# Performance work log

Hardware: AMD Instinct MI355X
Metric: run time of the kernel (lower is better)

Reference implementation:

```python
import jax, jax.numpy as jnp
import numpy as np

B, S, D_MODEL, D_HEAD = 8, 2048, 1024, 128
MAX_ROUNDS = 3
THRESH = 0.1
SCALE = 1.0 / np.sqrt(float(D_HEAD))


def setup_inputs() -> dict:
    key = jax.random.key(0)
    ks = jax.random.split(key, 12)

    def lin(k, out_d, in_d):
        # torch Linear weight layout [out, in], y = x @ W.T + b
        return (jax.random.normal(k, (out_d, in_d), jnp.float32) / np.sqrt(float(in_d))).astype(jnp.float32)

    thesis_w = lin(ks[3], D_HEAD, D_HEAD)
    return {
        "x": jax.random.normal(ks[0], (B, S, D_MODEL), jnp.float32),
        "wq": lin(ks[1], D_HEAD, D_MODEL),
        "wk": lin(ks[2], D_HEAD, D_MODEL),
        "wv": lin(ks[4], D_HEAD, D_MODEL),
        "thesis_w": thesis_w,  # antithesis weight is -thesis_w per __init__
        "thesis_b": 0.02 * jax.random.normal(ks[5], (D_HEAD,), jnp.float32),
        "anti_b": 0.02 * jax.random.normal(ks[6], (D_HEAD,), jnp.float32),
        "s_w1": lin(ks[7], D_HEAD, 3 * D_HEAD),
        "s_b1": jnp.zeros((D_HEAD,), jnp.float32),
        "s_w2": lin(ks[8], D_HEAD, D_HEAD),
        "s_b2": jnp.zeros((D_HEAD,), jnp.float32),
        "g_w": lin(ks[9], 1, 2 * D_HEAD),
        "g_b": jnp.zeros((1,), jnp.float32),
    }


def reference(x, wq, wk, wv, thesis_w, thesis_b, anti_b, s_w1, s_b1, s_w2, s_b2, g_w, g_b):
    # q/k/v projections (no bias)
    q = jnp.einsum("bsm,hm->bsh", x, wq)
    k = jnp.einsum("bsm,hm->bsh", x, wk)
    v = jnp.einsum("bsm,hm->bsh", x, wv)

    attn = jax.nn.softmax(jnp.einsum("bqh,bkh->bqk", q, k) * SCALE, axis=-1)
    # dropout is identity at eval time
    cur = jnp.einsum("bqk,bkh->bqh", attn, v)  # [B,S,Dh]

    # attn_weights and v never change across rounds, so thesis/antithesis are
    # round-invariant: compute the context projections once.
    context = cur
    thesis = context @ thesis_w.T + thesis_b
    anti = context @ (-thesis_w).T + anti_b  # antithesis weight = -thesis weight

    active = jnp.ones((B, S), dtype=bool)
    for _ in range(MAX_ROUNDS):
        # emulate `if not active_mask.any(): break` under jit
        any_active = jnp.any(active)
        am = active[..., None].astype(x.dtype)
        at, aa, ac = thesis * am, anti * am, cur * am

        h = jax.nn.relu(jnp.concatenate([at, aa, ac], axis=-1) @ s_w1.T + s_b1)
        synth = h @ s_w2.T + s_b2
        gate = jax.nn.sigmoid(jnp.concatenate([ac, synth], axis=-1) @ g_w.T + g_b)
        update = gate * (synth - ac) * 0.1
        new = cur + update  # applied to ALL tokens, matching original

        stable = jnp.linalg.norm(update, axis=-1) < THRESH  # new - cur == update
        cur = jnp.where(any_active, new, cur)
        active = jnp.where(any_active, active & ~stable, active)
    return cur
```

## Files before the change

### kernel.cpp

```cpp
#include <hip/hip_runtime.h>
#include <hip/hip_bf16.h>

#define B_   8
#define S_   2048
#define DM   1024
#define DH   128
#define BS_  16384
#define SCALE_  0.08838834764831845f
#define SCALE2_ 0.12751744f

typedef unsigned short u16;
typedef unsigned int   u32;
typedef _Float16 half8 __attribute__((ext_vector_type(8)));
typedef __bf16   bf16x8 __attribute__((ext_vector_type(8)));
typedef float    f32x4 __attribute__((ext_vector_type(4)));
typedef u32      u32x4 __attribute__((ext_vector_type(4)));

union H8 { u32x4 v; u32 u[4]; half8 h; bf16x8 b; };

__device__ __forceinline__ float bf2f(u16 u) {
    union { u32 i; float f; } w; w.i = ((u32)u) << 16; return w.f;
}
__device__ __forceinline__ void unpack8(uint4 v, float* f) {
    f[0] = bf2f(v.x & 0xffff); f[1] = bf2f(v.x >> 16);
    f[2] = bf2f(v.y & 0xffff); f[3] = bf2f(v.y >> 16);
    f[4] = bf2f(v.z & 0xffff); f[5] = bf2f(v.z >> 16);
    f[6] = bf2f(v.w & 0xffff); f[7] = bf2f(v.w >> 16);
}
__device__ __forceinline__ float ldE(const void* b, size_t i, int isbf16) {
    return isbf16 ? bf2f(((const u16*)b)[i]) : ((const float*)b)[i];
}
__device__ __forceinline__ void ld8(const void* b, size_t i, int isbf16, float* f) {
    if (isbf16) {
        unpack8(*(const uint4*)((const u16*)b + i), f);
    } else {
        float4 a = *(const float4*)((const float*)b + i);
        float4 c = *(const float4*)((const float*)b + i + 4);
        f[0] = a.x; f[1] = a.y; f[2] = a.z; f[3] = a.w;
        f[4] = c.x; f[5] = c.y; f[6] = c.z; f[7] = c.w;
    }
}
__device__ __forceinline__ u32 f2pk(float v) {
    _Float16 h = (_Float16)v;
    _Float16 l = (_Float16)(v - (float)h);
    union { _Float16 f; u16 u; } a, b; a.f = h; b.f = l;
    return ((u32)a.u << 16) | (u32)b.u;
}
__device__ __forceinline__ void split8(const float* f, u32x4& hi, u32x4& lo) {
    u32 H[8], L[8];
#pragma unroll
    for (int j = 0; j < 8; ++j) {
        _Float16 h = (_Float16)f[j];
        _Float16 l = (_Float16)(f[j] - (float)h);
        union { _Float16 x; u16 u; } a, b; a.x = h; b.x = l;
        H[j] = a.u; L[j] = b.u;
    }
    hi = (u32x4){H[0] | (H[1] << 16), H[2] | (H[3] << 16), H[4] | (H[5] << 16), H[6] | (H[7] << 16)};
    lo = (u32x4){L[0] | (L[1] << 16), L[2] | (L[3] << 16), L[4] | (L[5] << 16), L[6] | (L[7] << 16)};
}
__device__ __forceinline__ u32 permHI(u32 eB, u32 eA) { return __builtin_amdgcn_perm(eB, eA, 0x07060302u); }
__device__ __forceinline__ u16 f2h(float v) { union { _Float16 f; u16 u; } a; a.f = (_Float16)v; return a.u; }
__device__ __forceinline__ float h2f(u16 u) { union { _Float16 f; u16 u; } a; a.u = u; return (float)a.f; }

__global__ void init_kernel(const void* x, int* flag, int* active, int* counts) {
    int i = blockIdx.x * 256 + threadIdx.x;
    if (i < BS_) active[i] = 1;
    if (i < 4) counts[i] = (i == 0) ? BS_ : 0;
    if (i == 0) {
        const u16* w = (const u16*)x;
        int sane = 0;
        for (int t = 0; t < 256; ++t) {
            int e = (w[2 * t] >> 7) & 0xFF;
            if (e >= 100 && e <= 135) ++sane;
        }
        *flag = (sane >= 192) ? 1 : 0;
    }
}

__global__ __launch_bounds__(256) void prepack_w_kernel(
    const void* __restrict__ wq, const void* __restrict__ wk, const void* __restrict__ wv,
    const int* __restrict__ flag, u32x4* __restrict__ wpk)
{
    const int isb = *flag;
    const int gid = blockIdx.x * 256 + threadIdx.x;
    const int l  = gid & 63;
    const int t  = (gid >> 6) & 7;
    const int ks = (gid >> 9) & 31;
    const int z  = gid >> 14;
    const void* W = (z == 0) ? wq : (z == 1) ? wk : wv;
    const int row = 16 * t + (l & 15);
    const int k0  = ks * 32 + 8 * (l >> 4);
    const size_t base = ((((size_t)z * 32 + ks) * 16) + 2 * t) * 64 + l;
    if (isb) {
        uint4 v = *(const uint4*)((const u16*)W + (size_t)row * DM + k0);
        wpk[base] = (u32x4){v.x, v.y, v.z, v.w};
    } else {
        float f[8];
        ld8(W, (size_t)row * DM + k0, 0, f);
        u32x4 hi, lo;
        split8(f, hi, lo);
        wpk[base]      = hi;
        wpk[base + 64] = lo;
    }
}

__global__ __launch_bounds__(256) void qkv_kernel(
    const void* __restrict__ x, const u32x4* __restrict__ wpk,
    const int* __restrict__ flag, u32* __restrict__ qout,
    u32x4* __restrict__ kfrag, u32x4* __restrict__ vfrag)
{
    const int isb = *flag;
    const int z = blockIdx.z;
    const int bx = blockIdx.x;
    const int m0 = ((bx & 7) * 32 + (bx >> 3)) * 64;
    const int tid = threadIdx.x;
    const int wave = tid >> 6, lane = tid & 63;
    const int qd = lane >> 4, c = lane & 15;

    __shared__ u32x4 WLraw[2][16][64];
    u32x4 (*WLb)[2][8][64] = (u32x4(*)[2][8][64])WLraw;
    u32x4 (*WLf)[8][2][64] = (u32x4(*)[8][2][64])WLraw;
    u16 (*TS)[136] = (u16(*)[136])WLraw;

    const u32x4* wz = wpk + (size_t)z * (32 * 16 * 64);
    const size_t arow = (size_t)(m0 + wave * 16 + c) * DM + 8 * qd;

#define STAGE2(i_, b_)                                                            \
    {                                                                             \
        _Pragma("unroll")                                                         \
        for (int _j = 0; _j < 4; ++_j) {                                          \
            const int _g = wave * 4 + _j, _ksub = _g >> 3, _t = _g & 7;           \
            __builtin_amdgcn_global_load_lds(                                     \
                (const __attribute__((address_space(1))) u32*)(                   \
                    wz + ((size_t)(2 * (i_) + _ksub) * 16 + 2 * _t) * 64 + lane), \
                (__attribute__((address_space(3))) u32*)&WLb[b_][_ksub][_t][0],   \
                16, 0, 0);                                                        \
        }                                                                         \
    }
#define STAGE_W(ks_, b_)                                                          \
    {                                                                             \
        const u32x4* _src = wz + ((size_t)(ks_) * 16 + 4 * wave) * 64 + lane;     \
        _Pragma("unroll")                                                         \
        for (int _j = 0; _j < 4; ++_j) {                                          \
            __builtin_amdgcn_global_load_lds(                                     \
                (const __attribute__((address_space(1))) u32*)(_src + _j * 64),   \
                (__attribute__((address_space(3))) u32*)&WLf[b_][2 * wave + (_j >> 1)][_j & 1][0], \
                16, 0, 0);                                                        \
        }                                                                         \
    }

    f32x4 acc[8] = {};

    if (isb) {
        const u16* xb = (const u16*)x;
        uint4 A0 = *(const uint4*)(xb + arow);
        uint4 A1 = *(const uint4*)(xb + arow + 32);
        STAGE2(0, 0);
        uint4 A0n = *(const uint4*)(xb + arow + 64);
        uint4 A1n = *(const uint4*)(xb + arow + 96);
        __syncthreads();
        for (int i = 0; i < 16; ++i) {
            const int cb = i & 1;
            if (i + 1 < 16) STAGE2(i + 1, cb ^ 1);
            H8 Ah0; Ah0.v = (u32x4){A0.x, A0.y, A0.z, A0.w};
            H8 Ah1; Ah1.v = (u32x4){A1.x, A1.y, A1.z, A1.w};
#pragma unroll
            for (int t = 0; t < 8; ++t) {
                H8 bh; bh.v = WLb[cb][0][t][lane];
                acc[t] = __builtin_amdgcn_mfma_f32_16x16x32_bf16(Ah0.b, bh.b, acc[t], 0, 0, 0);
            }
#pragma unroll
            for (int t = 0; t < 8; ++t) {
                H8 bh; bh.v = WLb[cb][1][t][lane];
                acc[t] = __builtin_amdgcn_mfma_f32_16x16x32_bf16(Ah1.b, bh.b, acc[t], 0, 0, 0);
            }
            A0 = A0n; A1 = A1n;
            if (i + 2 < 16) {
                A0n = *(const uint4*)(xb + arow + (size_t)(i + 2) * 64);
                A1n = *(const uint4*)(xb + arow + (size_t)(i + 2) * 64 + 32);
            }
            __syncthreads();
        }
    } else {
        float Ar[8], Arn[8];
        ld8(x, arow, 0, Ar);
        STAGE_W(0, 0);
        ld8(x, arow + 32, 0, Arn);
        __syncthreads();
        for (int ks = 0; ks < 32; ++ks) {
            const int cb = ks & 1;
            if (ks + 1 < 32) STAGE_W(ks + 1, cb ^ 1);
            H8 Ah, Al;
            split8(Ar, Ah.v, Al.v);
#pragma unroll
            for (int t = 0; t < 8; ++t) {
                H8 bh, bl;
                bh.v = WLf[cb][t][0][lane]; bl.v = WLf[cb][t][1][lane];
                acc[t] = __builtin_amdgcn_mfma_f32_16x16x32_f16(Al.h, bh.h, acc[t], 0, 0, 0);
                acc[t] = __builtin_amdgcn_mfma_f32_16x16x32_f16(Ah.h, bl.h, acc[t], 0, 0, 0);
                acc[t] = __builtin_amdgcn_mfma_f32_16x16x32_f16(Ah.h, bh.h, acc[t], 0, 0, 0);
            }
#pragma unroll
            for (int j = 0; j < 8; ++j) Ar[j] = Arn[j];
            if (ks + 2 < 32) ld8(x, arow + (size_t)(ks + 2) * 32, 0, Arn);
            __syncthreads();
        }
    }
#undef STAGE2
#undef STAGE_W

    if (z == 0) {
#pragma unroll
        for (int r = 0; r < 4; ++r) {
            const int row = m0 + wave * 16 + qd * 4 + r;
            u32* op = qout + (size_t)row * DH + c;
#pragma unroll
            for (int t = 0; t < 8; ++t) op[t * 16] = f2pk(acc[t][r]);
        }
    } else {
#pragma unroll
        for (int t = 0; t < 8; ++t)
#pragma unroll
            for (int r = 0; r < 4; ++r)
                TS[wave * 16 + qd * 4 + r][16 * t + c] = f2h(acc[t][r]);
        __syncthreads();
        if (z == 1) {
#pragma unroll
            for (int i = 0; i < 4; ++i) {
                const int f = tid + 256 * i;
                const int lf = f & 63, ks = (f >> 6) & 3, sub = f >> 8;
                const int key = sub * 16 + (lf & 15);
                const int d0  = ks * 32 + 8 * (lf >> 4);
                u32 w[4];
#pragma unroll
                for (int q = 0; q < 4; ++q)
                    w[q] = (u32)TS[key][d0 + 2 * q] | ((u32)TS[key][d0 + 2 * q + 1] << 16);
                kfrag[((size_t)(m0 / 16 + sub) * 4 + ks) * 64 + lf] = (u32x4){w[0], w[1], w[2], w[3]};
            }
        } else {
#pragma unroll
            for (int i = 0; i < 4; ++i) {
                const int f = tid + 256 * i;
                const int lf = f & 63, t = (f >> 6) & 7, sub = f >> 9;
                const int kb2 = sub * 32 + 8 * (lf >> 4);
                const int dh  = 16 * t + (lf & 15);
                u32 w[4];
#pragma unroll
                for (int q = 0; q < 4; ++q)
                    w[q] = (u32)TS[kb2 + 2 * q][dh] | ((u32)TS[kb2 + 2 * q + 1][dh] << 16);
                vfrag[((size_t)(m0 / 32 + sub) * 8 + t) * 64 + lf] = (u32x4){w[0], w[1], w[2], w[3]};
            }
        }
    }
}

template <bool WRITE_PARTIAL>
__device__ __forceinline__ void attn_body(
    const u32* qp, const u32x4* __restrict__ kfrag, const u32x4* __restrict__ vfrag,
    u16* outO, u16* outL, float* cur,
    int b, int q0, int kt0, int kt1, int part)
{
    const int tid = threadIdx.x;
    const int wave = tid >> 6, lane = tid & 63;
    const int qd = lane >> 4, c = lane & 15;

    __shared__ u16 PB[4][531];

    H8 Qh[4];
    {
        const u32* qr = qp + ((size_t)b * S_ + q0 + wave * 16 + c) * DH;
#pragma unroll
        for (int ks = 0; ks < 4; ++ks) {
            uint4 e0 = *(const uint4*)(qr + ks * 32 + qd * 8);
            uint4 e1 = *(const uint4*)(qr + ks * 32 + qd * 8 + 4);
            Qh[ks].u[0] = permHI(e0.y, e0.x); Qh[ks].u[1] = permHI(e0.w, e0.z);
            Qh[ks].u[2] = permHI(e1.y, e1.x); Qh[ks].u[3] = permHI(e1.w, e1.z);
        }
    }

    f32x4 O[8] = {};
    float lsum[4] = {};

    const u32x4* kb0 = kfrag + (size_t)b * 128 * 256;
    const u32x4* vb0 = vfrag + (size_t)b * 64 * 512;

    for (int kt = kt0; kt < kt1; ++kt) {
        const u32x4* kf = kb0 + (size_t)kt * 512;
        const u32x4* vf = vb0 + (size_t)kt * 512;

        f32x4 S0 = {}, S1 = {};
#pragma unroll
        for (int ks = 0; ks < 4; ++ks) {
            H8 kh;
            kh.v = kf[ks * 64 + lane];
            S0 = __builtin_amdgcn_mfma_f32_16x16x32_f16(Qh[ks].h, kh.h, S0, 0, 0, 0);
            kh.v = kf[256 + ks * 64 + lane];
            S1 = __builtin_amdgcn_mfma_f32_16x16x32_f16(Qh[ks].h, kh.h, S1, 0, 0, 0);
        }

        u16* pw = PB[wave];
#pragma unroll
        for (int r = 0; r < 4; ++r) {
            float e0 = exp2f(fmaf(S0[r], SCALE2_, -4.0f));
            float e1 = exp2f(fmaf(S1[r], SCALE2_, -4.0f));
            lsum[r] += e0 + e1;
            pw[(4 * qd + r) * 33 + c]      = f2h(e0);
            pw[(4 * qd + r) * 33 + 16 + c] = f2h(e1);
        }

        u16 e[8];
#pragma unroll
        for (int j = 0; j < 8; ++j) e[j] = pw[c * 33 + 8 * qd + j];
        H8 Ph;
        Ph.u[0] = (u32)e[0] | ((u32)e[1] << 16);
        Ph.u[1] = (u32)e[2] | ((u32)e[3] << 16);
        Ph.u[2] = (u32)e[4] | ((u32)e[5] << 16);
        Ph.u[3] = (u32)e[6] | ((u32)e[7] << 16);

#pragma unroll
        for (int t = 0; t < 8; ++t) {
            H8 vh;
            vh.v = vf[t * 64 + lane];
            O[t] = __builtin_amdgcn_mfma_f32_16x16x32_f16(Ph.h, vh.h, O[t], 0, 0, 0);
        }
    }

    if (WRITE_PARTIAL) {
        float lred[4];
#pragma unroll
        for (int r = 0; r < 4; ++r) {
            float l = lsum[r];
            l += __shfl_xor(l, 1); l += __shfl_xor(l, 2);
            l += __shfl_xor(l, 4); l += __shfl_xor(l, 8);
            lred[r] = l;
        }
        const size_t rb = (size_t)b * S_ + q0 + wave * 16 + 4 * qd;
        u16* Op = outO + (size_t)part * ((size_t)BS_ * DH);
#pragma unroll
        for (int t = 0; t < 8; ++t)
#pragma unroll
            for (int r = 0; r < 4; ++r)
                Op[(rb + r) * DH + t * 16 + c] = f2h(O[t][r]);
        if (c == 0) {
            u16* lp = outL + (size_t)part * BS_;
#pragma unroll
            for (int r = 0; r < 4; ++r) lp[rb + r] = f2h(lred[r]);
        }
    } else {
        float linv[4];
#pragma unroll
        for (int r = 0; r < 4; ++r) {
            float l = lsum[r];
            l += __shfl_xor(l, 1); l += __shfl_xor(l, 2);
            l += __shfl_xor(l, 4); l += __shfl_xor(l, 8);
            linv[r] = 1.0f / l;
        }
        const size_t rb = (size_t)b * S_ + q0 + wave * 16 + 4 * qd;
#pragma unroll
        for (int t = 0; t < 8; ++t)
#pragma unroll
            for (int r = 0; r < 4; ++r)
                cur[(rb + r) * DH + t * 16 + c] = O[t][r] * linv[r];
    }
}

__global__ __launch_bounds__(256) void attn_kernel(
    const u32* qp, const u32x4* __restrict__ kfrag, const u32x4* __restrict__ vfrag, float* cur)
{
    const int rid = blockIdx.x + 32 * blockIdx.y;
    attn_body<false>(qp, kfrag, vfrag, nullptr, nullptr, cur,
                     rid & 7, ((rid >> 3) & 31) * 64, 0, S_ / 32, 0);
}

__global__ __launch_bounds__(256) void attn_split_kernel(
    const u32* qp, const u32x4* __restrict__ kfrag, const u32x4* __restrict__ vfrag,
    u16* __restrict__ Opart, u16* __restrict__ lpart)
{
    const int rid = blockIdx.x + 32 * (blockIdx.y + 8 * blockIdx.z);
    const int b    = rid & 7;
    const int qx   = (rid >> 3) & 31;
    const int part = rid >> 8;
    const int quart = S_ / 128;
    attn_body<true>(qp, kfrag, vfrag, Opart, lpart, nullptr,
                    b, qx * 64, part * quart, (part + 1) * quart, part);
}

__global__ __launch_bounds__(256) void combine_kernel(
    const u16* __restrict__ Opart, const u16* __restrict__ lpart,
    float* __restrict__ cur)
{
    const size_t N1 = (size_t)BS_ * DH;
    const size_t i0 = ((size_t)blockIdx.x * 256 + threadIdx.x) * 16;
    const int row = (int)(i0 >> 7);
    const float lt = h2f(lpart[row]) + h2f(lpart[BS_ + row])
                   + h2f(lpart[2 * BS_ + row]) + h2f(lpart[3 * BS_ + row]);
    const float linv = 1.0f / lt;
    float acc[16] = {};
#pragma unroll
    for (int p = 0; p < 4; ++p) {
        const u16* op = Opart + (size_t)p * N1 + i0;
        uint4 v0 = *(const uint4*)op;
        uint4 v1 = *(const uint4*)(op + 8);
        const u32 w[8] = {v0.x, v0.y, v0.z, v0.w, v1.x, v1.y, v1.z, v1.w};
#pragma unroll
        for (int j = 0; j < 8; ++j) {
            acc[2 * j]     += h2f((u16)(w[j] & 0xffff));
            acc[2 * j + 1] += h2f((u16)(w[j] >> 16));
        }
    }
#pragma unroll
    for (int t = 0; t < 4; ++t)
        *(float4*)(cur + i0 + t * 4) = make_float4(
            acc[4*t] * linv, acc[4*t+1] * linv, acc[4*t+2] * linv, acc[4*t+3] * linv);
}

__global__ __launch_bounds__(256) void prepack_rw_kernel(
    const void* __restrict__ tw, const void* __restrict__ w1, const void* __restrict__ w2,
    const int* __restrict__ flag, u32x4* __restrict__ pk)
{
    const int isb = *flag;
    const int gid = blockIdx.x * 256 + threadIdx.x;
    const int l = gid & 63, t = (gid >> 6) & 7, ks = (gid >> 9) & 3, mat = gid >> 11;
    const int row = 16 * t + (l & 15);
    const int k0  = ks * 32 + 8 * (l >> 4);
    float f[8];
    if (mat == 0)      ld8(tw, (size_t)row * DH + k0, isb, f);
    else if (mat <= 3) ld8(w1, (size_t)row * 384 + (mat - 1) * 128 + k0, isb, f);
    else               ld8(w2, (size_t)row * DH + k0, isb, f);
    u32x4 hi, lo;
    split8(f, hi, lo);
    const size_t base = (((size_t)mat * 4 + ks) * 16 + 2 * t) * 64 + l;
    pk[base] = hi; pk[base + 64] = lo;
}

struct Afrag { H8 h[4], l[4]; };
__device__ __forceinline__ void splitA(const float (&A)[4][8], Afrag& F) {
#pragma unroll
    for (int ks = 0; ks < 4; ++ks) split8(A[ks], F.h[ks].v, F.l[ks].v);
}

__global__ __launch_bounds__(256) void round_kernel(
    const float* cur0, const float* curr,
    const u32x4* __restrict__ pk,
    const void* __restrict__ tb, const void* __restrict__ ab,
    const void* __restrict__ b1, const void* __restrict__ b2,
    const void* __restrict__ gw, const void* __restrict__ gb,
    const int* __restrict__ flag, int* active, int* counts, int r,
    float* cur_out, void* dout)
{
    const int isb = *flag;
    const int tok0 = blockIdx.x * 32;
    const int tid = threadIdx.x;
    const bool last = (dout != nullptr);

    if (counts[r] <= 0) {
        if (last) {
            for (int e = tid; e < 32 * DH; e += 256) {
                size_t idx = (size_t)tok0 * DH + e;
                float v = curr[idx];
                if (isb) ((__hip_bfloat16*)dout)[idx] = __float2bfloat16(v);
                else     ((float*)dout)[idx] = v;
            }
        }
        return;
    }

    const int wave = tid >> 6, lane = tid & 63;
    const int qd = lane >> 4, c = lane & 15;
    const int rowg = wave >> 1, colh = wave & 1;

    __shared__ u32x4 WB[2][4][8][64];
    __shared__ u16 TS[32][132];
    __shared__ float actS[32], tbS[128], abS[128], b1S[128], b2S[128], gwS[256];
    __shared__ int blkcnt;

    auto stageB = [&](int mat, int buf) {
#pragma unroll
        for (int j = 0; j < 8; ++j) {
            const int g = wave * 8 + j, ks = g >> 3, t = g & 7;
            __builtin_amdgcn_global_load_lds(
                (const __attribute__((address_space(1))) u32*)(
                    pk + (((size_t)mat * 4 + ks) * 16 + 2 * t) * 64 + lane),
                (__attribute__((address_space(3))) u32*)&WB[buf][ks][t][0],
                16, 0, 0);
        }
    };
    auto stageF = [&](int mat, int h, int buf) {
#pragma unroll
        for (int j = 0; j < 8; ++j) {
            const int g = wave * 8 + j, kl = g >> 4, p = (g >> 3) & 1, t = g & 7;
            __builtin_amdgcn_global_load_lds(
                (const __attribute__((address_space(1))) u32*)(
                    pk + (((size_t)mat * 4 + 2 * h + kl) * 16 + 2 * t + p) * 64 + lane),
                (__attribute__((address_space(3))) u32*)&WB[buf][kl * 2 + p][t][0],
                16, 0, 0);
        }
    };
    auto gemmB = [&](const Afrag& F, int buf, f32x4 (&acc)[4]) {
#pragma unroll
        for (int ks = 0; ks < 4; ++ks)
#pragma unroll
            for (int tl = 0; tl < 4; ++tl) {
                H8 bh; bh.v = WB[buf][ks][4 * colh + tl][lane];
                acc[tl] = __builtin_amdgcn_mfma_f32_16x16x32_f16(F.l[ks].h, bh.h, acc[tl], 0, 0, 0);
                acc[tl] = __builtin_amdgcn_mfma_f32_16x16x32_f16(F.h[ks].h, bh.h, acc[tl], 0, 0, 0);
            }
    };
    auto gemmFh = [&](const Afrag& F, int h, int buf, f32x4 (&acc)[4]) {
#pragma unroll
        for (int kl = 0; kl < 2; ++kl) {
            const int ks = 2 * h + kl;
#pragma unroll
            for (int tl = 0; tl < 4; ++tl) {
                H8 bh, bl;
                bh.v = WB[buf][kl * 2][4 * colh + tl][lane];
                bl.v = WB[buf][kl * 2 + 1][4 * colh + tl][lane];
                acc[tl] = __builtin_amdgcn_mfma_f32_16x16x32_f16(F.l[ks].h, bh.h, acc[tl], 0, 0, 0);
                acc[tl] = __builtin_amdgcn_mfma_f32_16x16x32_f16(F.h[ks].h, bl.h, acc[tl], 0, 0, 0);
                acc[tl] = __builtin_amdgcn_mfma_f32_16x16x32_f16(F.h[ks].h, bh.h, acc[tl], 0, 0, 0);
            }
        }
    };
    auto STAGE = [&](int mat, int buf) { if (isb) stageB(mat, buf); else stageF(mat, 0, buf); };
    auto GEMM = [&](int mat, const Afrag& F, int buf, f32x4 (&acc)[4]) {
        if (isb) {
            gemmB(F, buf, acc);
        } else {
            gemmFh(F, 0, buf, acc);
            __syncthreads();
            stageF(mat, 1, buf);
            __syncthreads();
            gemmFh(F, 1, buf, acc);
        }
    };

    STAGE(0, 0);
    if (tid < 32) actS[tid] = active[tok0 + tid] ? 1.0f : 0.0f;
    if (tid < 128) {
        tbS[tid] = ldE(tb, tid, isb); abS[tid] = ldE(ab, tid, isb);
        b1S[tid] = ldE(b1, tid, isb); b2S[tid] = ldE(b2, tid, isb);
    }
    gwS[tid] = ldE(gw, tid, isb);
    if (tid == 0) blkcnt = 0;
    const float gbf = ldE(gb, 0, isb);

    const int rowl = 16 * rowg + c;
    const int hr   = 16 * rowg + 4 * qd;

    float A1[4][8];
    {
        const float* cr = cur0 + (size_t)(tok0 + rowl) * DH;
#pragma unroll
        for (int ks = 0; ks < 4; ++ks) {
            *(float4*)&A1[ks][0] = *(const float4*)(cr + ks * 32 + 8 * qd);
            *(float4*)&A1[ks][4] = *(const float4*)(cr + ks * 32 + 8 * qd + 4);
        }
    }
    Afrag FA; splitA(A1, FA);
    __syncthreads();

    STAGE(1, 1);
    {
        f32x4 accT[4] = {};
        GEMM(0, FA, 0, accT);
#pragma unroll
        for (int tl = 0; tl < 4; ++tl)
#pragma unroll
            for (int rr = 0; rr < 4; ++rr)
                TS[hr + rr][16 * (4 * colh + tl) + c] = f2h(accT[tl][rr]);
    }
    __syncthreads();

    STAGE(2, 0);
    f32x4 acc1[4] = {};
    const float am_r = actS[rowl];
    {
        float Ac[4][8];
#pragma unroll
        for (int ks = 0; ks < 4; ++ks)
#pragma unroll
            for (int j = 0; j < 8; ++j) {
                const int k = ks * 32 + 8 * qd + j;
                Ac[ks][j] = (h2f(TS[rowl][k]) + tbS[k]) * am_r;
            }
        Afrag FC; splitA(Ac, FC);
        GEMM(1, FC, 1, acc1);
    }
    __syncthreads();

    STAGE(3, 1);
    {
        float Ac[4][8];
#pragma unroll
        for (int ks = 0; ks < 4; ++ks)
#pragma unroll
            for (int j = 0; j < 8; ++j) {
                const int k = ks * 32 + 8 * qd + j;
                Ac[ks][j] = (abS[k] - h2f(TS[rowl][k])) * am_r;
            }
        Afrag FC; splitA(Ac, FC);
        GEMM(2, FC, 0, acc1);
    }
    __syncthreads();

    STAGE(4, 0);
    {
        float Ac[4][8];
        const float* cr = curr + (size_t)(tok0 + rowl) * DH;
#pragma unroll
        for (int ks = 0; ks < 4; ++ks) {
            float4 a0 = *(const float4*)(cr + ks * 32 + 8 * qd);
            float4 a1 = *(const float4*)(cr + ks * 32 + 8 * qd + 4);
            Ac[ks][0] = a0.x * am_r; Ac[ks][1] = a0.y * am_r;
            Ac[ks][2] = a0.z * am_r; Ac[ks][3] = a0.w * am_r;
            Ac[ks][4] = a1.x * am_r; Ac[ks][5] = a1.y * am_r;
            Ac[ks][6] = a1.z * am_r; Ac[ks][7] = a1.w * am_r;
        }
        Afrag FC; splitA(Ac, FC);
        GEMM(3, FC, 1, acc1);
    }
#pragma unroll
    for (int tl = 0; tl < 4; ++tl)
#pragma unroll
        for (int rr = 0; rr < 4; ++rr) {
            const int col = 16 * (4 * colh + tl) + c;
            TS[hr + rr][col] = f2h(fmaxf(acc1[tl][rr] + b1S[col], 0.0f));
        }
    __syncthreads();

    {
        float Ac[4][8];
#pragma unroll
        for (int ks = 0; ks < 4; ++ks)
#pragma unroll
            for (int j = 0; j < 8; ++j)
                Ac[ks][j] = h2f(TS[rowl][ks * 32 + 8 * qd + j]);
        Afrag FC; splitA(Ac, FC);
        f32x4 acc2[4] = {};
        GEMM(4, FC, 0, acc2);
        __syncthreads();
#pragma unroll
        for (int tl = 0; tl < 4; ++tl)
#pragma unroll
            for (int rr = 0; rr < 4; ++rr) {
                const int col = 16 * (4 * colh + tl) + c;
                TS[hr + rr][col] = f2h(acc2[tl][rr] + b2S[col]);
            }
    }
    __syncthreads();

    const int tok = tid >> 3, d0 = (tid & 7) * 16;
    const float am = actS[tok];
    const float* cp = curr + (size_t)(tok0 + tok) * DH + d0;
    float cv[16];
#pragma unroll
    for (int t = 0; t < 4; ++t) {
        float4 vv = *(const float4*)(cp + t * 4);
        cv[t * 4] = vv.x; cv[t * 4 + 1] = vv.y; cv[t * 4 + 2] = vv.z; cv[t * 4 + 3] = vv.w;
    }
    float srow[16];
#pragma unroll
    for (int e = 0; e < 16; ++e) srow[e] = h2f(TS[tok][d0 + e]);
    float gp = 0.0f;
#pragma unroll
    for (int e = 0; e < 16; ++e)
        gp += cv[e] * am * gwS[d0 + e] + srow[e] * gwS[128 + d0 + e];
    gp += __shfl_xor(gp, 1, 8);
    gp += __shfl_xor(gp, 2, 8);
    gp += __shfl_xor(gp, 4, 8);
    const float gate = 1.0f / (1.0f + __expf(-(gp + gbf)));
    float ss = 0.0f; float up[16];
#pragma unroll
    for (int e = 0; e < 16; ++e) {
        float u = gate * (srow[e] - cv[e] * am) * 0.1f;
        up[e] = u; ss += u * u;
    }
    ss += __shfl_xor(ss, 1, 8);
    ss += __shfl_xor(ss, 2, 8);
    ss += __shfl_xor(ss, 4, 8);
    const bool stable = sqrtf(ss) < 0.1f;

    if (last) {
        size_t off = (size_t)(tok0 + tok) * DH + d0;
        if (isb) {
            __hip_bfloat16* op = (__hip_bfloat16*)dout + off;
#pragma unroll
            for (int e = 0; e < 16; ++e) op[e] = __float2bfloat16(cv[e] + up[e]);
        } else {
            float* op = (float*)dout + off;
#pragma unroll
            for (int t = 0; t < 4; ++t)
                *(float4*)(op + t * 4) = make_float4(cv[t * 4] + up[t * 4], cv[t * 4 + 1] + up[t * 4 + 1],
                                                     cv[t * 4 + 2] + up[t * 4 + 2], cv[t * 4 + 3] + up[t * 4 + 3]);
        }
    } else {
        float* op = cur_out + (size_t)(tok0 + tok) * DH + d0;
#pragma unroll
        for (int t = 0; t < 4; ++t)
            *(float4*)(op + t * 4) = make_float4(cv[t * 4] + up[t * 4], cv[t * 4 + 1] + up[t * 4 + 1],
                                                 cv[t * 4 + 2] + up[t * 4 + 2], cv[t * 4 + 3] + up[t * 4 + 3]);
    }
    const int newact = (am > 0.0f && !stable) ? 1 : 0;
    if ((tid & 7) == 0) {
        active[tok0 + tok] = newact;
        if (newact) atomicAdd(&blkcnt, 1);
    }
    __syncthreads();
    if (tid == 0 && blkcnt > 0) atomicAdd(&counts[r + 1], blkcnt);
}

extern "C" void kernel_launch(void* const* d_in, const int* in_sizes, int n_in,
                              void* d_out, int out_size, void* d_ws, size_t ws_size,
                              hipStream_t stream) {
    const void* x  = d_in[0];
    const void* wq = d_in[1];
    const void* wk = d_in[2];
    const void* wv = d_in[3];
    const void* tw = d_in[4];
    const void* tb = d_in[5];
    const void* ab = d_in[6];
    const void* w1 = d_in[7];
    const void* b1 = d_in[8];
    const void* w2 = d_in[9];
    const void* b2 = d_in[10];
    const void* gw = d_in[11];
    const void* gb = d_in[12];

    u32* ws = (u32*)d_ws;
    const size_t N1 = (size_t)BS_ * DH;
    u32* qp = ws;
    u32* kp = ws + N1;
    u32* vp = ws + 2 * N1;
    int* active = (int*)(ws + 3 * N1);
    int* counts = active + BS_;
    int* flag   = counts + 4;
    float* cur0  = (float*)qp;
    float* cur_r = (float*)kp;
    u16* Opart16 = (u16*)(ws + 3 * N1 + 32768);
    u16* lpart16 = (u16*)(ws + 5 * N1 + 32768);
    const bool big_ws = ws_size >= (size_t)42300000;
    u32x4* wpk = (u32x4*)(ws + 3 * N1 + 32768);
    u32x4* pkRW = (u32x4*)vp;
    u32x4* kfragP = (u32x4*)kp;
    u32x4* vfragP = (u32x4*)vp;

    init_kernel<<<dim3(BS_ / 256), 256, 0, stream>>>(x, flag, active, counts);
    prepack_w_kernel<<<dim3(192), 256, 0, stream>>>(wq, wk, wv, flag, wpk);
    qkv_kernel<<<dim3(BS_ / 64, 1, 3), 256, 0, stream>>>(x, wpk, flag, qp, kfragP, vfragP);
    if (big_ws) {
        attn_split_kernel<<<dim3(S_ / 64, B_, 4), 256, 0, stream>>>(qp, kfragP, vfragP, Opart16, lpart16);
        combine_kernel<<<dim3(512), 256, 0, stream>>>(Opart16, lpart16, cur0);
    } else {
        attn_kernel<<<dim3(S_ / 64, B_), 256, 0, stream>>>(qp, kfragP, vfragP, cur0);
    }
    prepack_rw_kernel<<<dim3(40), 256, 0, stream>>>(tw, w1, w2, flag, pkRW);
    round_kernel<<<dim3(BS_ / 32), 256, 0, stream>>>(
        cur0, cur0, pkRW, tb, ab, b1, b2, gw, gb, flag, active, counts, 0, cur_r, nullptr);
    round_kernel<<<dim3(BS_ / 32), 256, 0, stream>>>(
        cur0, cur_r, pkRW, tb, ab, b1, b2, gw, gb, flag, active, counts, 1, cur_r, nullptr);
    round_kernel<<<dim3(BS_ / 32), 256, 0, stream>>>(
        cur0, cur_r, pkRW, tb, ab, b1, b2, gw, gb, flag, active, counts, 2, cur_r, d_out);
}
```

Before: 256.5 us.

## Load QKV weight fragments directly from global into registers, drop LDS staging

Removes the double-buffered global_load_lds staging of packed weight fragments and the per-iteration __syncthreads in the QKV projection kernel. Each wave now reads its B fragments straight from global memory (L2) into registers, with software register prefetch in the bf16 path and no prefetch in the fp32 split path. This removes barrier and LDS traffic, but every wave in a block now fetches the same weights redundantly from cache. It also raises register pressure, and the fp32 path loses latency hiding for its loads.

Result: slower. 287.3 us (+12.0%).

```diff
diff --git a/kernel.cpp b/kernel.cpp
--- a/kernel.cpp
+++ b/kernel.cpp
@@ -117,97 +117,55 @@
     const int wave = tid >> 6, lane = tid & 63;
     const int qd = lane >> 4, c = lane & 15;
 
-    __shared__ u32x4 WLraw[2][16][64];
-    u32x4 (*WLb)[2][8][64] = (u32x4(*)[2][8][64])WLraw;
-    u32x4 (*WLf)[8][2][64] = (u32x4(*)[8][2][64])WLraw;
-    u16 (*TS)[136] = (u16(*)[136])WLraw;
+    __shared__ u16 TS[64][136];
 
     const u32x4* wz = wpk + (size_t)z * (32 * 16 * 64);
     const size_t arow = (size_t)(m0 + wave * 16 + c) * DM + 8 * qd;
 
-#define STAGE2(i_, b_)                                                            \
-    {                                                                             \
-        _Pragma("unroll")                                                         \
-        for (int _j = 0; _j < 4; ++_j) {                                          \
-            const int _g = wave * 4 + _j, _ksub = _g >> 3, _t = _g & 7;           \
-            __builtin_amdgcn_global_load_lds(                                     \
-                (const __attribute__((address_space(1))) u32*)(                   \
-                    wz + ((size_t)(2 * (i_) + _ksub) * 16 + 2 * _t) * 64 + lane), \
-                (__attribute__((address_space(3))) u32*)&WLb[b_][_ksub][_t][0],   \
-                16, 0, 0);                                                        \
-        }                                                                         \
-    }
-#define STAGE_W(ks_, b_)                                                          \
-    {                                                                             \
-        const u32x4* _src = wz + ((size_t)(ks_) * 16 + 4 * wave) * 64 + lane;     \
-        _Pragma("unroll")                                                         \
-        for (int _j = 0; _j < 4; ++_j) {                                          \
-            __builtin_amdgcn_global_load_lds(                                     \
-                (const __attribute__((address_space(1))) u32*)(_src + _j * 64),   \
-                (__attribute__((address_space(3))) u32*)&WLf[b_][2 * wave + (_j >> 1)][_j & 1][0], \
-                16, 0, 0);                                                        \
-        }                                                                         \
-    }
-
     f32x4 acc[8] = {};
 
     if (isb) {
         const u16* xb = (const u16*)x;
-        uint4 A0 = *(const uint4*)(xb + arow);
-        uint4 A1 = *(const uint4*)(xb + arow + 32);
-        STAGE2(0, 0);
-        uint4 A0n = *(const uint4*)(xb + arow + 64);
-        uint4 A1n = *(const uint4*)(xb + arow + 96);
-        __syncthreads();
-        for (int i = 0; i < 16; ++i) {
-            const int cb = i & 1;
-            if (i + 1 < 16) STAGE2(i + 1, cb ^ 1);
-            H8 Ah0; Ah0.v = (u32x4){A0.x, A0.y, A0.z, A0.w};
-            H8 Ah1; Ah1.v = (u32x4){A1.x, A1.y, A1.z, A1.w};
-#pragma unroll
-            for (int t = 0; t < 8; ++t) {
-                H8 bh; bh.v = WLb[cb][0][t][lane];
-                acc[t] = __builtin_amdgcn_mfma_f32_16x16x32_bf16(Ah0.b, bh.b, acc[t], 0, 0, 0);
-            }
-#pragma unroll
-            for (int t = 0; t < 8; ++t) {
-                H8 bh; bh.v = WLb[cb][1][t][lane];
-                acc[t] = __builtin_amdgcn_mfma_f32_16x16x32_bf16(Ah1.b, bh.b, acc[t], 0, 0, 0);
-            }
-            A0 = A0n; A1 = A1n;
-            if (i + 2 < 16) {
-                A0n = *(const uint4*)(xb + arow + (size_t)(i + 2) * 64);
-                A1n = *(const uint4*)(xb + arow + (size_t)(i + 2) * 64 + 32);
-            }
-            __syncthreads();
+        uint4 Ab = *(const uint4*)(xb + arow);
+        H8 Bc[8];
+#pragma unroll
+        for (int t = 0; t < 8; ++t) Bc[t].v = wz[(size_t)(2 * t) * 64 + lane];
+        for (int ks = 0; ks < 32; ++ks) {
+            H8 Bn[8];
+            uint4 An;
+            if (ks + 1 < 32) {
+#pragma unroll
+                for (int t = 0; t < 8; ++t)
+                    Bn[t].v = wz[((size_t)(ks + 1) * 16 + 2 * t) * 64 + lane];
+                An = *(const uint4*)(xb + arow + (size_t)(ks + 1) * 32);
+            }
+            H8 Ah; Ah.v = (u32x4){Ab.x, Ab.y, Ab.z, Ab.w};
+#pragma unroll
+            for (int t = 0; t < 8; ++t)
+                acc[t] = __builtin_amdgcn_mfma_f32_16x16x32_bf16(Ah.b, Bc[t].b, acc[t], 0, 0, 0);
+            if (ks + 1 < 32) {
+#pragma unroll
+                for (int t = 0; t < 8; ++t) Bc[t] = Bn[t];
+                Ab = An;
+            }
         }
     } else {
-        float Ar[8], Arn[8];
-        ld8(x, arow, 0, Ar);
-        STAGE_W(0, 0);
-        ld8(x, arow + 32, 0, Arn);
-        __syncthreads();
+        float Ar[8];
         for (int ks = 0; ks < 32; ++ks) {
-            const int cb = ks & 1;
-            if (ks + 1 < 32) STAGE_W(ks + 1, cb ^ 1);
+            ld8(x, arow + (size_t)ks * 32, 0, Ar);
             H8 Ah, Al;
             split8(Ar, Ah.v, Al.v);
 #pragma unroll
             for (int t = 0; t < 8; ++t) {
                 H8 bh, bl;
-                bh.v = WLf[cb][t][0][lane]; bl.v = WLf[cb][t][1][lane];
+                bh.v = wz[((size_t)ks * 16 + 2 * t) * 64 + lane];
+                bl.v = wz[((size_t)ks * 16 + 2 * t + 1) * 64 + lane];
                 acc[t] = __builtin_amdgcn_mfma_f32_16x16x32_f16(Al.h, bh.h, acc[t], 0, 0, 0);
                 acc[t] = __builtin_amdgcn_mfma_f32_16x16x32_f16(Ah.h, bl.h, acc[t], 0, 0, 0);
                 acc[t] = __builtin_amdgcn_mfma_f32_16x16x32_f16(Ah.h, bh.h, acc[t], 0, 0, 0);
             }
-#pragma unroll
-            for (int j = 0; j < 8; ++j) Ar[j] = Arn[j];
-            if (ks + 2 < 32) ld8(x, arow + (size_t)(ks + 2) * 32, 0, Arn);
-            __syncthreads();
-        }
-    }
-#undef STAGE2
-#undef STAGE_W
+        }
+    }
 
     if (z == 0) {
 #pragma unroll
```

## Halve QKV block row tile and split output columns across waves

Applied to the files above, without the earlier changes.

The QKV projection kernel now processes 32 rows per block instead of 64. The four waves form a 2x2 grid over rows and the two 64-column halves, and the grid is doubled to match. Each wave keeps half as many accumulators, which lowers register pressure and doubles the number of blocks to improve occupancy and load balance. In exchange, the weight tiles staged in LDS are reused across fewer rows, so global weight traffic per output roughly doubles.

Result: slower. 298.9 us (+16.5%).

```diff
diff --git a/kernel.cpp b/kernel.cpp
--- a/kernel.cpp
+++ b/kernel.cpp
@@ -112,10 +112,11 @@
     const int isb = *flag;
     const int z = blockIdx.z;
     const int bx = blockIdx.x;
-    const int m0 = ((bx & 7) * 32 + (bx >> 3)) * 64;
+    const int m0 = ((bx & 7) * 64 + (bx >> 3)) * 32;
     const int tid = threadIdx.x;
     const int wave = tid >> 6, lane = tid & 63;
     const int qd = lane >> 4, c = lane & 15;
+    const int rowg = wave >> 1, colh = wave & 1;
 
     __shared__ u32x4 WLraw[2][16][64];
     u32x4 (*WLb)[2][8][64] = (u32x4(*)[2][8][64])WLraw;
@@ -123,7 +124,8 @@
     u16 (*TS)[136] = (u16(*)[136])WLraw;
 
     const u32x4* wz = wpk + (size_t)z * (32 * 16 * 64);
-    const size_t arow = (size_t)(m0 + wave * 16 + c) * DM + 8 * qd;
+    const int rowl = 16 * rowg + c;
+    const size_t arow = (size_t)(m0 + rowl) * DM + 8 * qd;
 
 #define STAGE2(i_, b_)                                                            \
     {                                                                             \
@@ -149,7 +151,7 @@
         }                                                                         \
     }
 
-    f32x4 acc[8] = {};
+    f32x4 acc[4] = {};
 
     if (isb) {
         const u16* xb = (const u16*)x;
@@ -165,14 +167,14 @@
             H8 Ah0; Ah0.v = (u32x4){A0.x, A0.y, A0.z, A0.w};
             H8 Ah1; Ah1.v = (u32x4){A1.x, A1.y, A1.z, A1.w};
 #pragma unroll
-            for (int t = 0; t < 8; ++t) {
-                H8 bh; bh.v = WLb[cb][0][t][lane];
-                acc[t] = __builtin_amdgcn_mfma_f32_16x16x32_bf16(Ah0.b, bh.b, acc[t], 0, 0, 0);
-            }
-#pragma unroll
-            for (int t = 0; t < 8; ++t) {
-                H8 bh; bh.v = WLb[cb][1][t][lane];
-                acc[t] = __builtin_amdgcn_mfma_f32_16x16x32_bf16(Ah1.b, bh.b, acc[t], 0, 0, 0);
+            for (int tl = 0; tl < 4; ++tl) {
+                H8 bh; bh.v = WLb[cb][0][4 * colh + tl][lane];
+                acc[tl] = __builtin_amdgcn_mfma_f32_16x16x32_bf16(Ah0.b, bh.b, acc[tl], 0, 0, 0);
+            }
+#pragma unroll
+            for (int tl = 0; tl < 4; ++tl) {
+                H8 bh; bh.v = WLb[cb][1][4 * colh + tl][lane];
+                acc[tl] = __builtin_amdgcn_mfma_f32_16x16x32_bf16(Ah1.b, bh.b, acc[tl], 0, 0, 0);
             }
             A0 = A0n; A1 = A1n;
             if (i + 2 < 16) {
@@ -193,12 +195,13 @@
             H8 Ah, Al;
             split8(Ar, Ah.v, Al.v);
 #pragma unroll
-            for (int t = 0; t < 8; ++t) {
+            for (int tl = 0; tl < 4; ++tl) {
                 H8 bh, bl;
-                bh.v = WLf[cb][t][0][lane]; bl.v = WLf[cb][t][1][lane];
-                acc[t] = __builtin_amdgcn_mfma_f32_16x16x32_f16(Al.h, bh.h, acc[t], 0, 0, 0);
-                acc[t] = __builtin_amdgcn_mfma_f32_16x16x32_f16(Ah.h, bl.h, acc[t], 0, 0, 0);
-                acc[t] = __builtin_amdgcn_mfma_f32_16x16x32_f16(Ah.h, bh.h, acc[t], 0, 0, 0);
+                bh.v = WLf[cb][4 * colh + tl][0][lane];
+                bl.v = WLf[cb][4 * colh + tl][1][lane];
+                acc[tl] = __builtin_amdgcn_mfma_f32_16x16x32_f16(Al.h, bh.h, acc[tl], 0, 0, 0);
+                acc[tl] = __builtin_amdgcn_mfma_f32_16x16x32_f16(Ah.h, bl.h, acc[tl], 0, 0, 0);
+                acc[tl] = __builtin_amdgcn_mfma_f32_16x16x32_f16(Ah.h, bh.h, acc[tl], 0, 0, 0);
             }
 #pragma unroll
             for (int j = 0; j < 8; ++j) Ar[j] = Arn[j];
@@ -212,21 +215,21 @@
     if (z == 0) {
 #pragma unroll
         for (int r = 0; r < 4; ++r) {
-            const int row = m0 + wave * 16 + qd * 4 + r;
-            u32* op = qout + (size_t)row * DH + c;
-#pragma unroll
-            for (int t = 0; t < 8; ++t) op[t * 16] = f2pk(acc[t][r]);
+            const int row = m0 + 16 * rowg + 4 * qd + r;
+            u32* op = qout + (size_t)row * DH + 64 * colh + c;
+#pragma unroll
+            for (int tl = 0; tl < 4; ++tl) op[tl * 16] = f2pk(acc[tl][r]);
         }
     } else {
 #pragma unroll
-        for (int t = 0; t < 8; ++t)
+        for (int tl = 0; tl < 4; ++tl)
 #pragma unroll
             for (int r = 0; r < 4; ++r)
-                TS[wave * 16 + qd * 4 + r][16 * t + c] = f2h(acc[t][r]);
+                TS[16 * rowg + 4 * qd + r][16 * (4 * colh + tl) + c] = f2h(acc[tl][r]);
         __syncthreads();
         if (z == 1) {
 #pragma unroll
-            for (int i = 0; i < 4; ++i) {
+            for (int i = 0; i < 2; ++i) {
                 const int f = tid + 256 * i;
                 const int lf = f & 63, ks = (f >> 6) & 3, sub = f >> 8;
                 const int key = sub * 16 + (lf & 15);
@@ -239,16 +242,16 @@
             }
         } else {
 #pragma unroll
-            for (int i = 0; i < 4; ++i) {
+            for (int i = 0; i < 2; ++i) {
                 const int f = tid + 256 * i;
-                const int lf = f & 63, t = (f >> 6) & 7, sub = f >> 9;
-                const int kb2 = sub * 32 + 8 * (lf >> 4);
+                const int lf = f & 63, t = (f >> 6) & 7;
+                const int kb2 = 8 * (lf >> 4);
                 const int dh  = 16 * t + (lf & 15);
                 u32 w[4];
 #pragma unroll
                 for (int q = 0; q < 4; ++q)
                     w[q] = (u32)TS[kb2 + 2 * q][dh] | ((u32)TS[kb2 + 2 * q + 1][dh] << 16);
-                vfrag[((size_t)(m0 / 32 + sub) * 8 + t) * 64 + lf] = (u32x4){w[0], w[1], w[2], w[3]};
+                vfrag[((size_t)(m0 / 32) * 8 + t) * 64 + lf] = (u32x4){w[0], w[1], w[2], w[3]};
             }
         }
     }
@@ -746,7 +749,7 @@
 
     init_kernel<<<dim3(BS_ / 256), 256, 0, stream>>>(x, flag, active, counts);
     prepack_w_kernel<<<dim3(192), 256, 0, stream>>>(wq, wk, wv, flag, wpk);
-    qkv_kernel<<<dim3(BS_ / 64, 1, 3), 256, 0, stream>>>(x, wpk, flag, qp, kfragP, vfragP);
+    qkv_kernel<<<dim3(BS_ / 32, 1, 3), 256, 0, stream>>>(x, wpk, flag, qp, kfragP, vfragP);
     if (big_ws) {
         attn_split_kernel<<<dim3(S_ / 64, B_, 4), 256, 0, stream>>>(qp, kfragP, vfragP, Opart16, lpart16);
         combine_kernel<<<dim3(512), 256, 0, stream>>>(Opart16, lpart16, cur0);
```

## Cache round-invariant thesis projection across rounds and vectorize attention P transpose

Applied to the files above, without the earlier changes.

The first round kernel stores the thesis projection (context @ thesis_w) to a workspace buffer as fp16, and later rounds reload it instead of recomputing that GEMM. This removes one of the per-round GEMMs in rounds 1 and 2. In the attention kernel, the P scratch row stride changes from 33 to 40 so each lane reads its fragment with a single 16-byte LDS load instead of eight 2-byte loads, and s_setprio is raised around the MFMA loops. The wider stride may add LDS bank conflicts on the writes. The cached buffer also reuses part of the v-fragment workspace region, which must not overlap live data.

Measured after the change: 254.7 us. About the same (-0.7%).

```diff
diff --git a/kernel.cpp b/kernel.cpp
--- a/kernel.cpp
+++ b/kernel.cpp
@@ -264,7 +264,7 @@
     const int wave = tid >> 6, lane = tid & 63;
     const int qd = lane >> 4, c = lane & 15;
 
-    __shared__ u16 PB[4][531];
+    __shared__ __align__(16) u16 PB[4][640];
 
     H8 Qh[4];
     {
@@ -289,6 +289,7 @@
         const u32x4* vf = vb0 + (size_t)kt * 512;
 
         f32x4 S0 = {}, S1 = {};
+        __builtin_amdgcn_s_setprio(1);
 #pragma unroll
         for (int ks = 0; ks < 4; ++ks) {
             H8 kh;
@@ -297,6 +298,7 @@
             kh.v = kf[256 + ks * 64 + lane];
             S1 = __builtin_amdgcn_mfma_f32_16x16x32_f16(Qh[ks].h, kh.h, S1, 0, 0, 0);
         }
+        __builtin_amdgcn_s_setprio(0);
 
         u16* pw = PB[wave];
 #pragma unroll
@@ -304,25 +306,22 @@
             float e0 = exp2f(fmaf(S0[r], SCALE2_, -4.0f));
             float e1 = exp2f(fmaf(S1[r], SCALE2_, -4.0f));
             lsum[r] += e0 + e1;
-            pw[(4 * qd + r) * 33 + c]      = f2h(e0);
-            pw[(4 * qd + r) * 33 + 16 + c] = f2h(e1);
-        }
-
-        u16 e[8];
-#pragma unroll
-        for (int j = 0; j < 8; ++j) e[j] = pw[c * 33 + 8 * qd + j];
+            pw[(4 * qd + r) * 40 + c]      = f2h(e0);
+            pw[(4 * qd + r) * 40 + 16 + c] = f2h(e1);
+        }
+
+        uint4 ev = *(const uint4*)&pw[c * 40 + 8 * qd];
         H8 Ph;
-        Ph.u[0] = (u32)e[0] | ((u32)e[1] << 16);
-        Ph.u[1] = (u32)e[2] | ((u32)e[3] << 16);
-        Ph.u[2] = (u32)e[4] | ((u32)e[5] << 16);
-        Ph.u[3] = (u32)e[6] | ((u32)e[7] << 16);
-
+        Ph.u[0] = ev.x; Ph.u[1] = ev.y; Ph.u[2] = ev.z; Ph.u[3] = ev.w;
+
+        __builtin_amdgcn_s_setprio(1);
 #pragma unroll
         for (int t = 0; t < 8; ++t) {
             H8 vh;
             vh.v = vf[t * 64 + lane];
             O[t] = __builtin_amdgcn_mfma_f32_16x16x32_f16(Ph.h, vh.h, O[t], 0, 0, 0);
         }
+        __builtin_amdgcn_s_setprio(0);
     }
 
     if (WRITE_PARTIAL) {
@@ -441,7 +440,7 @@
 
 __global__ __launch_bounds__(256) void round_kernel(
     const float* cur0, const float* curr,
-    const u32x4* __restrict__ pk,
+    const u32x4* __restrict__ pk, u16* __restrict__ T0,
     const void* __restrict__ tb, const void* __restrict__ ab,
     const void* __restrict__ b1, const void* __restrict__ b2,
     const void* __restrict__ gw, const void* __restrict__ gb,
@@ -534,7 +533,7 @@
         }
     };
 
-    STAGE(0, 0);
+    if (r == 0) STAGE(0, 0); else STAGE(1, 1);
     if (tid < 32) actS[tid] = active[tok0 + tid] ? 1.0f : 0.0f;
     if (tid < 128) {
         tbS[tid] = ldE(tb, tid, isb); abS[tid] = ldE(ab, tid, isb);
@@ -547,20 +546,26 @@
     const int rowl = 16 * rowg + c;
     const int hr   = 16 * rowg + 4 * qd;
 
-    float A1[4][8];
-    {
+    Afrag FA;
+    if (r == 0) {
+        float A1[4][8];
         const float* cr = cur0 + (size_t)(tok0 + rowl) * DH;
 #pragma unroll
         for (int ks = 0; ks < 4; ++ks) {
             *(float4*)&A1[ks][0] = *(const float4*)(cr + ks * 32 + 8 * qd);
             *(float4*)&A1[ks][4] = *(const float4*)(cr + ks * 32 + 8 * qd + 4);
         }
-    }
-    Afrag FA; splitA(A1, FA);
+        splitA(A1, FA);
+    } else {
+        for (int i = tid; i < 32 * 64; i += 256) {
+            const int row = i >> 6, c2 = (i & 63) * 2;
+            *(u32*)&TS[row][c2] = *(const u32*)&T0[(size_t)(tok0 + row) * DH + c2];
+        }
+    }
     __syncthreads();
 
-    STAGE(1, 1);
-    {
+    if (r == 0) {
+        STAGE(1, 1);
         f32x4 accT[4] = {};
         GEMM(0, FA, 0, accT);
 #pragma unroll
@@ -568,8 +573,12 @@
 #pragma unroll
             for (int rr = 0; rr < 4; ++rr)
                 TS[hr + rr][16 * (4 * colh + tl) + c] = f2h(accT[tl][rr]);
-    }
-    __syncthreads();
+        __syncthreads();
+        for (int i = tid; i < 32 * 64; i += 256) {
+            const int row = i >> 6, c2 = (i & 63) * 2;
+            *(u32*)&T0[(size_t)(tok0 + row) * DH + c2] = *(const u32*)&TS[row][c2];
+        }
+    }
 
     STAGE(2, 0);
     f32x4 acc1[4] = {};
@@ -741,6 +750,7 @@
     const bool big_ws = ws_size >= (size_t)42300000;
     u32x4* wpk = (u32x4*)(ws + 3 * N1 + 32768);
     u32x4* pkRW = (u32x4*)vp;
+    u16*   T0c  = (u16*)(vp + 131072);
     u32x4* kfragP = (u32x4*)kp;
     u32x4* vfragP = (u32x4*)vp;
 
@@ -755,9 +765,9 @@
     }
     prepack_rw_kernel<<<dim3(40), 256, 0, stream>>>(tw, w1, w2, flag, pkRW);
     round_kernel<<<dim3(BS_ / 32), 256, 0, stream>>>(
-        cur0, cur0, pkRW, tb, ab, b1, b2, gw, gb, flag, active, counts, 0, cur_r, nullptr);
+        cur0, cur0, pkRW, T0c, tb, ab, b1, b2, gw, gb, flag, active, counts, 0, cur_r, nullptr);
     round_kernel<<<dim3(BS_ / 32), 256, 0, stream>>>(
-        cur0, cur_r, pkRW, tb, ab, b1, b2, gw, gb, flag, active, counts, 1, cur_r, nullptr);
+        cur0, cur_r, pkRW, T0c, tb, ab, b1, b2, gw, gb, flag, active, counts, 1, cur_r, nullptr);
     round_kernel<<<dim3(BS_ / 32), 256, 0, stream>>>(
-        cur0, cur_r, pkRW, tb, ab, b1, b2, gw, gb, flag, active, counts, 2, cur_r, d_out);
-}
+        cur0, cur_r, pkRW, T0c, tb, ab, b1, b2, gw, gb, flag, active, counts, 2, cur_r, d_out);
+}
```
